# Optimization experiments

Hardware: AMD Instinct MI355X
Metric: run time of the kernel (lower is better)

Reference implementation:

```python
import jax, jax.numpy as jnp
import numpy as np

N, C, T, V, O, S, R = 32, 64, 256, 25, 192, 3, 8  # batch, in_ch, time, joints, out_ch, subsets, rel_ch


def setup_inputs() -> dict:
    key = jax.random.key(0)
    ks = jax.random.split(key, 20)
    w = lambda i, shape: (jax.random.normal(ks[i], shape, jnp.float32) * 0.05)
    return {
        "x": jax.random.normal(ks[0], (N, C, T, V), jnp.float32),
        "spd_A": jax.random.normal(ks[1], (V, V), jnp.float32) * 0.1,
        "A3": jax.random.normal(ks[2], (S, V, V), jnp.float32) * 0.1,
        "A6": jax.random.normal(ks[3], (6, V, V), jnp.float32) * 0.1,
        "conv1_w": w(4, (S, R, C)), "conv1_b": jnp.zeros((S, R), jnp.float32),
        "conv2_w": w(5, (S, R, C)), "conv2_b": jnp.zeros((S, R), jnp.float32),
        "conv4_w": w(6, (S, O, R)), "conv4_b": jnp.zeros((S, O), jnp.float32),
        "conv3_w": w(7, (S, O, C)), "conv3_b": jnp.zeros((S, O), jnp.float32),
        "alpha": jnp.full((1,), 0.5, jnp.float32),
        "beta": jnp.full((1,), 0.5, jnp.float32),
        "gamma": jnp.full((1,), 0.5, jnp.float32),
        "bn_w": jnp.ones((O,), jnp.float32), "bn_b": jnp.zeros((O,), jnp.float32),
        "down_w": w(8, (O, C)), "down_b": jnp.zeros((O,), jnp.float32),
        "dbn_w": jnp.ones((O,), jnp.float32), "dbn_b": jnp.zeros((O,), jnp.float32),
    }


def _bn(y, w, b):
    # BatchNorm2d in training mode: stats over (N, T, V) per channel, biased var
    mu = y.mean(axis=(0, 2, 3), keepdims=True)
    var = ((y - mu) ** 2).mean(axis=(0, 2, 3), keepdims=True)
    return (y - mu) * jax.lax.rsqrt(var + 1e-5) * w[None, :, None, None] + b[None, :, None, None]


def reference(x, spd_A, A3, A6, conv1_w, conv1_b, conv2_w, conv2_b, conv4_w, conv4_b,
              conv3_w, conv3_b, alpha, beta, gamma, bn_w, bn_b, down_w, down_b, dbn_w, dbn_b):
    out_c = conv4_w.shape[1]
    # A6 expanded: (out//6, 6, V, V) -> (out, V, V); contiguous-view == tile along channel blocks
    A6_ex = jnp.tile(A6, (out_c // 6, 1, 1))  # (O, V, V)
    # 1x1 conv then temporal mean == conv on temporal mean (linear op commutes)
    xm = x.mean(axis=2)  # (N, C, V)
    x1 = jnp.einsum('ncv,src->nsrv', xm, conv1_w) + conv1_b[None, :, :, None]
    x2 = jnp.einsum('ncv,src->nsrv', xm, conv2_w) + conv2_b[None, :, :, None]
    d = jnp.tanh(x1[..., :, None] - x2[..., None, :])  # (N, S, R, V, V)
    A_dyn = jnp.einsum('nsruv,sor->nsouv', d, conv4_w) + conv4_b[None, :, :, None, None]
    A_at = (A_dyn * alpha + A3[None, :, None, :, :]
            + A6_ex[None, None] * beta + spd_A[None, None, None] * gamma)  # (N, S, O, V, V)
    # CTRGC_2: x3 = conv3(x); einsum 'ncuv,nctv->nctu', summed over subsets
    x3 = jnp.einsum('nctv,soc->nsotv', x, conv3_w) + conv3_b[None, :, :, None, None]
    y = jnp.einsum('nsouv,nsotv->notu', A_at, x3)  # (N, O, T, V)
    y = _bn(y, bn_w, bn_b)
    xd = jnp.einsum('nctv,oc->notv', x, down_w) + down_b[None, :, None, None]
    y = jax.nn.relu(y + _bn(xd, dbn_w, dbn_b))
    return y
```

## Files before the change

kernel.cpp:

```cpp
#include <hip/hip_runtime.h>

#define N_ 32
#define C_ 64
#define T_ 256
#define V_ 25
#define O_ 192
#define S_ 3
#define R_ 8
#define VV (V_*V_)
#define TV (T_*V_)
#define RP 26
#define TRP (T_*RP)

typedef unsigned short u16;
typedef unsigned int u32;
typedef __attribute__((ext_vector_type(4))) u16 u16x4;
typedef __attribute__((ext_vector_type(8))) u16 u16x8;
typedef __attribute__((ext_vector_type(4))) u32 u32x4;
typedef __attribute__((ext_vector_type(8))) __bf16 bf16x8;
typedef __attribute__((ext_vector_type(4))) float f32x4;

#define WS_A2F_U 0
#define WS_XQ_U  (18874368)
#define WS_XD_U  (18874368 + 13631488)
#define WS_YB_U  (18874368 + 13631488 + 39321600)
#define WS_XM_F   (55574528)
#define WS_RS_F   (55574528 + 51200)
#define WS_STAT_F (55574528 + 51200 + 153600)
#define WS_COEF_F (55574528 + 51200 + 153600 + 768)

__device__ __forceinline__ u16 f2b(float f) {
    return __builtin_bit_cast(u16, (__bf16)f);
}
__device__ __forceinline__ float b2f(u16 u) {
    return __builtin_bit_cast(float, ((unsigned)u) << 16);
}
__device__ __forceinline__ f32x4 mfma16(bf16x8 a, bf16x8 b, f32x4 c) {
    return __builtin_amdgcn_mfma_f32_16x16x32_bf16(a, b, c, 0, 0, 0);
}

__global__ void k0_xq(const float* __restrict__ x, u16* __restrict__ xq) {
    __shared__ float tile[64][52];
    int bid = blockIdx.x;
    int n = bid >> 7, tb = bid & 127;
    int t0 = tb * 2;
    int tid = threadIdx.x;
    const float2* xp = (const float2*)(x + (size_t)n * C_ * TV + t0 * 25);
    for (int p = tid; p < 1600; p += 256) {
        int c = p / 25, q = p % 25;
        float2 f2 = xp[(size_t)c * 3200 + q];
        tile[c][q * 2] = f2.x;
        tile[c][q * 2 + 1] = f2.y;
    }
    __syncthreads();
    for (int p = tid; p < 832; p += 256) {
        int row = p >> 4, c4g = p & 15;
        int t = row >= RP, v = row - t * RP;
        u16x4 w;
        #pragma unroll
        for (int i = 0; i < 4; ++i) {
            int co = ((c4g & 3) << 4) + ((c4g >> 2) << 2) + i;
            w[i] = (v < 25) ? f2b(tile[co][t * 25 + v]) : (u16)0;
        }
        *(u16x4*)&xq[((size_t)n * TRP + tb * 52 + row) * 64 + c4g * 4] = w;
    }
}

__global__ void k1_xm(const u16* __restrict__ xq, float* __restrict__ xm_out) {
    __shared__ float ps[256];
    int bid = blockIdx.x;
    int n = bid / 25, v = bid % 25;
    int tid = threadIdx.x;
    int cg = tid & 63, tg = tid >> 6;
    const u16* p = xq + (size_t)n * TRP * 64 + ((size_t)(tg * 64 * RP + v)) * 64 + cg;
    float s = 0.f;
    for (int t = 0; t < 64; ++t) {
        s += b2f(*p);
        p += RP * 64;
    }
    ps[tid] = s;
    __syncthreads();
    if (tid < 64) {
        float tot = ps[tid] + ps[64 + tid] + ps[128 + tid] + ps[192 + tid];
        int c4g = tid >> 2, i = tid & 3;
        int co = ((c4g & 3) << 4) + ((c4g >> 2) << 2) + i;
        xm_out[((size_t)n * C_ + co) * V_ + v] = tot * (1.f / T_);
    }
}

__global__ void k2_a2f(const float* __restrict__ spd, const float* __restrict__ A3,
                       const float* __restrict__ A6,
                       const float* __restrict__ w1, const float* __restrict__ b1,
                       const float* __restrict__ w2, const float* __restrict__ b2,
                       const float* __restrict__ w4, const float* __restrict__ b4,
                       const float* __restrict__ b3,
                       const float* __restrict__ alpha, const float* __restrict__ beta,
                       const float* __restrict__ gamma,
                       u16* __restrict__ a2f, const float* __restrict__ xmbuf,
                       float* __restrict__ rs_tot) {
    __shared__ float xm[C_ * V_];
    __shared__ float x1s[R_ * V_], x2s[R_ * V_];
    __shared__ float dm[R_ * VV];
    __shared__ float a3s[VV], sps[VV], a6s[6 * VV];
    __shared__ float aat[2 * VV];
    __shared__ float w4s[2][R_];
    __shared__ float b4s[2];
    int bid = blockIdx.x;
    int n = bid / 24;
    int rem = bid % 24;
    int s = rem / 8, og = rem % 8;
    int tid = threadIdx.x;
    const float* xmg = xmbuf + (size_t)n * C_ * V_;
    for (int p = tid; p < C_ * V_; p += 256) xm[p] = xmg[p];
    for (int p = tid; p < VV; p += 256) { a3s[p] = A3[s * VV + p]; sps[p] = spd[p]; }
    for (int p = tid; p < 6 * VV; p += 256) a6s[p] = A6[p];
    __syncthreads();
    if (tid < R_ * V_) {
        int r = tid / V_, v = tid % V_;
        float acc1 = b1[s * R_ + r], acc2 = b2[s * R_ + r];
        for (int c = 0; c < C_; ++c) {
            float xv = xm[c * V_ + v];
            acc1 += xv * w1[(s * R_ + r) * C_ + c];
            acc2 += xv * w2[(s * R_ + r) * C_ + c];
        }
        x1s[tid] = acc1; x2s[tid] = acc2;
    }
    __syncthreads();
    for (int p = tid; p < R_ * VV; p += 256) {
        int r = p / VV, uv = p % VV, u = uv / V_, v = uv % V_;
        dm[p] = tanhf(x1s[r * V_ + u] - x2s[r * V_ + v]);
    }
    __syncthreads();
    float al = alpha[0], be = beta[0], ga = gamma[0];
    for (int op = 0; op < 12; ++op) {
        int o0 = og * 24 + op * 2;
        if (tid < 16) w4s[tid >> 3][tid & 7] =
            w4[((size_t)(s * O_ + o0 + (tid >> 3))) * R_ + (tid & 7)];
        if (tid < 2) b4s[tid] = b4[s * O_ + o0 + tid];
        __syncthreads();
        for (int p = tid; p < 2 * VV; p += 256) {
            int oo = p / VV, pp = p % VV;
            float acc = b4s[oo];
            #pragma unroll
            for (int r = 0; r < R_; ++r) acc += dm[r * VV + pp] * w4s[oo][r];
            int o = o0 + oo;
            aat[p] = al * acc + a3s[pp] + be * a6s[(o % 6) * VV + pp] + ga * sps[pp];
        }
        __syncthreads();
        if (tid < 2 * V_) {
            int oo = tid / V_, u = tid % V_;
            float rs = 0.f;
            for (int v = 0; v < V_; ++v) rs += aat[oo * VV + u * V_ + v];
            atomicAdd(&rs_tot[((size_t)(n * O_ + o0 + oo)) * V_ + u],
                      b3[s * O_ + o0 + oo] * rs);
        }
        {
            int oo = tid >> 7, l2 = tid & 127, cu = l2 >> 6, l = l2 & 63;
            int u = cu * 16 + (l & 15);
            u16x8 w;
            #pragma unroll
            for (int j = 0; j < 8; ++j) {
                int v = ((j >> 2) << 4) + ((l >> 4) << 2) + (j & 3);
                float val = 0.f;
                if (u < V_ && v < V_) val = aat[oo * VV + u * V_ + v];
                w[j] = f2b(val);
            }
            size_t idx = ((((size_t)(n * O_ + o0 + oo)) * S_ + s) * 2 + cu) * 64 + l;
            ((u16x8*)a2f)[idx] = w;
        }
        __syncthreads();
    }
}

#define OSTR_B 2504
#define SSTR_B 832
#define BUF_B  20064

__global__ __launch_bounds__(256, 3)
void k3_main(const u16* __restrict__ xq,
             const float* __restrict__ w3, const float* __restrict__ dw,
             const float* __restrict__ db,
             const u16* __restrict__ a2f, const float* __restrict__ rs_tot,
             u16* __restrict__ yb16, u16* __restrict__ xdws,
             float* __restrict__ stats) {
    __shared__ char x3Lb[2 * BUF_B];
    __shared__ u16 xdst[8 * 416];
    __shared__ u16 ystage[8 * 400];
    int orig = blockIdx.x;
    int bid = (orig & 7) * 96 + (orig >> 3);
    int n = bid / 24;
    int o0 = (bid % 24) * 8;
    int tid = threadIdx.x, wid = tid >> 6, lane = tid & 63;
    int lr = lane & 15, lg = lane >> 4;
    int colt = wid & 1;
    int rt0 = (wid >> 1) * 13;

    for (int p = tid; p < 2 * BUF_B / 16; p += 256) ((u32x4*)x3Lb)[p] = u32x4{0,0,0,0};

    const float* wsrc = (colt == 0)
        ? w3 + ((size_t)((lr >> 3) * O_ + o0 + (lr & 7))) * C_
        : ((lr < 8) ? w3 + ((size_t)(2 * O_ + o0 + lr)) * C_
                    : dw + ((size_t)(o0 + lr - 8)) * C_);
    bf16x8 bw[2];
    #pragma unroll
    for (int ks = 0; ks < 2; ++ks) {
        u16x8 tmp;
        #pragma unroll
        for (int j = 0; j < 8; ++j) {
            int c = ks * 32 + (lg << 2) + (j & 3) + ((j >> 2) << 4);
            tmp[j] = f2b(wsrc[c]);
        }
        bw[ks] = __builtin_bit_cast(bf16x8, tmp);
    }
    float dbv = (colt == 1 && lr >= 8) ? db[o0 + lr - 8] : 0.f;

    int wo = (colt == 0) ? (lr & 7) : lr;
    int wsb = (colt == 0) ? (lr >> 3) : 2;
    int colbyte = wo * OSTR_B + wsb * SSTR_B;

    const bf16x8* a2v = (const bf16x8*)a2f;
    bf16x8 Bh[2][6];
    float rsb0[2], rsb1[2];
    #pragma unroll
    for (int oi = 0; oi < 2; ++oi) {
        int o = o0 + (wid << 1) + oi;
        const bf16x8* bp = a2v + ((size_t)(n * O_ + o)) * 6 * 64 + lane;
        #pragma unroll
        for (int q = 0; q < 6; ++q) Bh[oi][q] = bp[(size_t)q * 64];
        const float* rsp = rs_tot + ((size_t)(n * O_ + o)) * V_;
        rsb0[oi] = rsp[lr];
        rsb1[oi] = (lr < 9) ? rsp[16 + lr] : 0.f;
    }

    float sy1[2] = {0, 0}, sy2[2] = {0, 0};
    float sd1 = 0.f, sd2 = 0.f;
    const u16* xbn = xq + (size_t)n * TRP * 64;
    int rdw = 13 * lr + 2 * lg;
    char* buf = x3Lb;
    int t0 = 0;

    auto tl = [&](int ch, int j, u16x8& A0, u16x8& A1) {
        const u16* p = xbn + ((size_t)(ch * 16) * RP + (size_t)((rt0 + j) * 16 + lr)) * 64
                       + (lg << 4);
        A0 = *(const u16x8*)p;
        A1 = *(const u16x8*)(p + 8);
    };
    auto proc = [&](int rt, u16x8 A0, u16x8 A1) {
        f32x4 acc = {0.f, 0.f, 0.f, 0.f};
        acc = mfma16(__builtin_bit_cast(bf16x8, A0), bw[0], acc);
        acc = mfma16(__builtin_bit_cast(bf16x8, A1), bw[1], acc);
        int rbase = rt * 16 + (lg << 2);
        if (colt == 0 || lr < 8) {
            u16x4 w;
            #pragma unroll
            for (int reg = 0; reg < 4; ++reg) w[reg] = f2b(acc[reg]);
            *(u16x4*)(buf + colbyte + rbase * 2) = w;
        } else {
            u16x4 w;
            #pragma unroll
            for (int reg = 0; reg < 4; ++reg) {
                int rr = rbase + reg;
                int t = rr / RP, v = rr - t * RP;
                float val = acc[reg] + dbv;
                w[reg] = f2b(val);
                if (v < 25) { sd1 += val; sd2 += val * val; }
            }
            *(u16x4*)&xdst[(lr - 8) * 416 + rbase] = w;
        }
    };

    __syncthreads();

    u16x8 p0a, p0b, p1a, p1b, p2a, p2b, p3a, p3b;
    tl(0, 0, p0a, p0b); tl(0, 1, p1a, p1b); tl(0, 2, p2a, p2b); tl(0, 3, p3a, p3b);

    for (int ch = 0; ch < 16; ++ch) {
        t0 = ch * 16;
        buf = x3Lb + (ch & 1) * BUF_B;
        proc(rt0 + 0, p0a, p0b);
        proc(rt0 + 1, p1a, p1b);
        proc(rt0 + 2, p2a, p2b);
        proc(rt0 + 3, p3a, p3b);
        for (int j = 4; j < 13; ++j) {
            u16x8 A0, A1;
            tl(ch, j, A0, A1);
            proc(rt0 + j, A0, A1);
        }
        if (ch < 15) {
            tl(ch + 1, 0, p0a, p0b); tl(ch + 1, 1, p1a, p1b);
            tl(ch + 1, 2, p2a, p2b); tl(ch + 1, 3, p3a, p3b);
        }
        __syncthreads();
        #pragma unroll
        for (int oi = 0; oi < 2; ++oi) {
            int ol = (wid << 1) + oi;
            const u32* L = (const u32*)(buf + ol * OSTR_B);
            f32x4 acc0 = {0, 0, 0, 0}, acc1 = {0, 0, 0, 0};
            #pragma unroll
            for (int s = 0; s < 3; ++s) {
                const u32* Ls = L + s * 208 + rdw;
                u32 d0 = Ls[0], d1 = Ls[1], d8 = Ls[8], d9 = Ls[9];
                bf16x8 A = __builtin_bit_cast(bf16x8, u32x4{d0, d1, d8, d9});
                acc0 = mfma16(A, Bh[oi][s * 2 + 0], acc0);
                acc1 = mfma16(A, Bh[oi][s * 2 + 1], acc1);
            }
            int ylb = ol * 400 + (lg << 2) * 25;
            #pragma unroll
            for (int reg = 0; reg < 4; ++reg) {
                float v0 = acc0[reg] + rsb0[oi];
                ystage[ylb + reg * 25 + lr] = f2b(v0);
                sy1[oi] += v0; sy2[oi] += v0 * v0;
                if (lr < 9) {
                    float v1 = acc1[reg] + rsb1[oi];
                    ystage[ylb + reg * 25 + 16 + lr] = f2b(v1);
                    sy1[oi] += v1; sy2[oi] += v1 * v1;
                }
            }
        }
        {
            size_t ygb = (size_t)(n * O_ + o0) * TV + (size_t)t0 * V_;
            for (int q = lane; q < 100; q += 64) {
                int sel = q >= 50;
                int ol2 = (wid << 1) + sel;
                int j = q - sel * 50;
                u16x8 pk = *(const u16x8*)&ystage[ol2 * 400 + j * 8];
                *(u16x8*)&yb16[ygb + (size_t)ol2 * TV + j * 8] = pk;
            }
        }
        if (colt == 1) {
            int tofs = (wid >> 1) * 8;
            size_t gdb = (size_t)(n * O_ + o0) * TV + (size_t)(t0 + tofs) * V_;
            for (int q = lane; q < 200; q += 64) {
                int o = q / 25, w = q - o * 25;
                int g0 = w * 8;
                int tl2 = g0 / 25, v = g0 - tl2 * 25;
                u16x8 pk;
                #pragma unroll
                for (int k = 0; k < 8; ++k) {
                    pk[k] = xdst[o * 416 + (tofs + tl2) * RP + v];
                    if (++v == 25) { v = 0; ++tl2; }
                }
                *(u16x8*)&xdws[gdb + (size_t)o * TV + g0] = pk;
            }
        }
    }
    #pragma unroll
    for (int oi = 0; oi < 2; ++oi) {
        float v1 = sy1[oi], v2 = sy2[oi];
        #pragma unroll
        for (int m = 1; m < 64; m <<= 1) {
            v1 += __shfl_xor(v1, m);
            v2 += __shfl_xor(v2, m);
        }
        if (lane == 0) {
            atomicAdd(&stats[0 * O_ + o0 + (wid << 1) + oi], v1);
            atomicAdd(&stats[1 * O_ + o0 + (wid << 1) + oi], v2);
        }
    }
    if (colt == 1) {
        float v1 = sd1, v2 = sd2;
        v1 += __shfl_xor(v1, 16); v2 += __shfl_xor(v2, 16);
        v1 += __shfl_xor(v1, 32); v2 += __shfl_xor(v2, 32);
        if (lane >= 8 && lane < 16) {
            atomicAdd(&stats[2 * O_ + o0 + lane - 8], v1);
            atomicAdd(&stats[3 * O_ + o0 + lane - 8], v2);
        }
    }
}

__global__ void k4_coef(const float* __restrict__ bn_w, const float* __restrict__ bn_b,
                        const float* __restrict__ dbn_w, const float* __restrict__ dbn_b,
                        const float* __restrict__ stats, float* __restrict__ coef) {
    int o = threadIdx.x;
    if (o >= O_) return;
    float inv = 1.f / (float)(N_ * T_ * V_);
    float mu_y = stats[o] * inv;
    float var_y = stats[O_ + o] * inv - mu_y * mu_y;
    float ay = bn_w[o] * rsqrtf(var_y + 1e-5f);
    float by = bn_b[o] - mu_y * ay;
    float mu_d = stats[2 * O_ + o] * inv;
    float var_d = stats[3 * O_ + o] * inv - mu_d * mu_d;
    float ad = dbn_w[o] * rsqrtf(var_d + 1e-5f);
    float bd = dbn_b[o] - mu_d * ad;
    coef[o] = ay; coef[O_ + o] = by; coef[2 * O_ + o] = ad; coef[3 * O_ + o] = bd;
}

__global__ void k5_final(float* __restrict__ out, const u16* __restrict__ yb,
                         const u16* __restrict__ xd, const float* __restrict__ cf) {
    size_t total = (size_t)N_ * O_ * TV / 8;
    for (size_t i = blockIdx.x * (size_t)blockDim.x + threadIdx.x; i < total;
         i += (size_t)gridDim.x * blockDim.x) {
        int o = (int)((i / 800) % O_);
        float ay = cf[o], by = cf[O_ + o], ad = cf[2 * O_ + o], bd = cf[3 * O_ + o];
        u16x8 yv = ((const u16x8*)yb)[i];
        u16x8 dv = ((const u16x8*)xd)[i];
        float4 r0, r1;
        r0.x = fmaxf(ay * b2f(yv[0]) + by + ad * b2f(dv[0]) + bd, 0.f);
        r0.y = fmaxf(ay * b2f(yv[1]) + by + ad * b2f(dv[1]) + bd, 0.f);
        r0.z = fmaxf(ay * b2f(yv[2]) + by + ad * b2f(dv[2]) + bd, 0.f);
        r0.w = fmaxf(ay * b2f(yv[3]) + by + ad * b2f(dv[3]) + bd, 0.f);
        r1.x = fmaxf(ay * b2f(yv[4]) + by + ad * b2f(dv[4]) + bd, 0.f);
        r1.y = fmaxf(ay * b2f(yv[5]) + by + ad * b2f(dv[5]) + bd, 0.f);
        r1.z = fmaxf(ay * b2f(yv[6]) + by + ad * b2f(dv[6]) + bd, 0.f);
        r1.w = fmaxf(ay * b2f(yv[7]) + by + ad * b2f(dv[7]) + bd, 0.f);
        ((float4*)out)[2 * i] = r0;
        ((float4*)out)[2 * i + 1] = r1;
    }
}

extern "C" void kernel_launch(void* const* d_in, const int* in_sizes, int n_in,
                              void* d_out, int out_size, void* d_ws, size_t ws_size,
                              hipStream_t stream) {
    const float* x     = (const float*)d_in[0];
    const float* spd   = (const float*)d_in[1];
    const float* A3    = (const float*)d_in[2];
    const float* A6    = (const float*)d_in[3];
    const float* w1    = (const float*)d_in[4];
    const float* b1    = (const float*)d_in[5];
    const float* w2    = (const float*)d_in[6];
    const float* b2    = (const float*)d_in[7];
    const float* w4    = (const float*)d_in[8];
    const float* b4    = (const float*)d_in[9];
    const float* w3    = (const float*)d_in[10];
    const float* b3    = (const float*)d_in[11];
    const float* alpha = (const float*)d_in[12];
    const float* beta  = (const float*)d_in[13];
    const float* gamma = (const float*)d_in[14];
    const float* bn_w  = (const float*)d_in[15];
    const float* bn_b  = (const float*)d_in[16];
    const float* dw    = (const float*)d_in[17];
    const float* db    = (const float*)d_in[18];
    const float* dbn_w = (const float*)d_in[19];
    const float* dbn_b = (const float*)d_in[20];
    float* out = (float*)d_out;
    u16*   wsu = (u16*)d_ws;
    float* wsf = (float*)d_ws;

    u16* a2f  = wsu + WS_A2F_U;
    u16* xq   = wsu + WS_XQ_U;
    u16* xd   = wsu + WS_XD_U;
    u16* yb   = wsu + WS_YB_U;
    float* xm    = wsf + WS_XM_F;
    float* rs    = wsf + WS_RS_F;
    float* stats = wsf + WS_STAT_F;
    float* coef  = wsf + WS_COEF_F;

    hipMemsetAsync(rs, 0, (N_ * O_ * V_ + 4 * O_) * sizeof(float), stream);

    k0_xq<<<N_ * 128, 256, 0, stream>>>(x, xq);
    k1_xm<<<N_ * 25, 256, 0, stream>>>(xq, xm);
    k2_a2f<<<N_ * S_ * 8, 256, 0, stream>>>(spd, A3, A6, w1, b1, w2, b2, w4, b4, b3,
                                            alpha, beta, gamma, a2f, xm, rs);
    k3_main<<<N_ * 24, 256, 0, stream>>>(xq, w3, dw, db, a2f, rs, yb, xd, stats);
    k4_coef<<<1, 256, 0, stream>>>(bn_w, bn_b, dbn_w, dbn_b, stats, coef);
    k5_final<<<4096, 256, 0, stream>>>(out, yb, xd, coef);
}
```

Baseline: 315.4 us.

## Split main kernel time range across two blocks and make a2f per-wave

```diff
diff --git a/kernel.cpp b/kernel.cpp
--- a/kernel.cpp
+++ b/kernel.cpp
@@ -101,19 +101,16 @@
     __shared__ float xm[C_ * V_];
     __shared__ float x1s[R_ * V_], x2s[R_ * V_];
     __shared__ float dm[R_ * VV];
-    __shared__ float a3s[VV], sps[VV], a6s[6 * VV];
-    __shared__ float aat[2 * VV];
-    __shared__ float w4s[2][R_];
-    __shared__ float b4s[2];
+    __shared__ float a3s[VV], sps[VV];
+    __shared__ float aatw[4][2 * VV];
     int bid = blockIdx.x;
     int n = bid / 24;
     int rem = bid % 24;
     int s = rem / 8, og = rem % 8;
-    int tid = threadIdx.x;
+    int tid = threadIdx.x, wid = tid >> 6, lane = tid & 63;
     const float* xmg = xmbuf + (size_t)n * C_ * V_;
     for (int p = tid; p < C_ * V_; p += 256) xm[p] = xmg[p];
     for (int p = tid; p < VV; p += 256) { a3s[p] = A3[s * VV + p]; sps[p] = spd[p]; }
-    for (int p = tid; p < 6 * VV; p += 256) a6s[p] = A6[p];
     __syncthreads();
     if (tid < R_ * V_) {
         int r = tid / V_, v = tid % V_;
@@ -132,30 +129,37 @@
     }
     __syncthreads();
     float al = alpha[0], be = beta[0], ga = gamma[0];
-    for (int op = 0; op < 12; ++op) {
+    float* aat = aatw[wid];
+    for (int opi = 0; opi < 3; ++opi) {
+        int op = wid * 3 + opi;
         int o0 = og * 24 + op * 2;
-        if (tid < 16) w4s[tid >> 3][tid & 7] =
-            w4[((size_t)(s * O_ + o0 + (tid >> 3))) * R_ + (tid & 7)];
-        if (tid < 2) b4s[tid] = b4[s * O_ + o0 + tid];
-        __syncthreads();
-        for (int p = tid; p < 2 * VV; p += 256) {
-            int oo = p / VV, pp = p % VV;
-            float acc = b4s[oo];
-            #pragma unroll
-            for (int r = 0; r < R_; ++r) acc += dm[r * VV + pp] * w4s[oo][r];
-            int o = o0 + oo;
-            aat[p] = al * acc + a3s[pp] + be * a6s[(o % 6) * VV + pp] + ga * sps[pp];
-        }
-        __syncthreads();
-        if (tid < 2 * V_) {
-            int oo = tid / V_, u = tid % V_;
+        float w4v[2][R_], b4v[2];
+        #pragma unroll
+        for (int oo = 0; oo < 2; ++oo) {
+            b4v[oo] = b4[s * O_ + o0 + oo];
+            #pragma unroll
+            for (int r = 0; r < R_; ++r)
+                w4v[oo][r] = w4[((size_t)(s * O_ + o0 + oo)) * R_ + r];
+        }
+        const float* a6p0 = A6 + ((o0 % 6) * VV);
+        for (int p = lane; p < 2 * VV; p += 64) {
+            int oo = p / VV, pp = p - oo * VV;
+            float acc = b4v[oo];
+            #pragma unroll
+            for (int r = 0; r < R_; ++r) acc += dm[r * VV + pp] * w4v[oo][r];
+            aat[p] = al * acc + a3s[pp] + ga * sps[pp] + be * a6p0[oo * VV + pp];
+        }
+        if (lane < 2 * V_) {
+            int oo = lane / V_, u = lane - oo * V_;
             float rs = 0.f;
             for (int v = 0; v < V_; ++v) rs += aat[oo * VV + u * V_ + v];
             atomicAdd(&rs_tot[((size_t)(n * O_ + o0 + oo)) * V_ + u],
                       b3[s * O_ + o0 + oo] * rs);
         }
-        {
-            int oo = tid >> 7, l2 = tid & 127, cu = l2 >> 6, l = l2 & 63;
+        #pragma unroll
+        for (int it = 0; it < 4; ++it) {
+            int idx = it * 64 + lane;
+            int oo = idx >> 7, l2 = idx & 127, cu = l2 >> 6, l = l2 & 63;
             int u = cu * 16 + (l & 15);
             u16x8 w;
             #pragma unroll
@@ -165,10 +169,9 @@
                 if (u < V_ && v < V_) val = aat[oo * VV + u * V_ + v];
                 w[j] = f2b(val);
             }
-            size_t idx = ((((size_t)(n * O_ + o0 + oo)) * S_ + s) * 2 + cu) * 64 + l;
-            ((u16x8*)a2f)[idx] = w;
-        }
-        __syncthreads();
+            size_t idxg = ((((size_t)(n * O_ + o0 + oo)) * S_ + s) * 2 + cu) * 64 + l;
+            ((u16x8*)a2f)[idxg] = w;
+        }
     }
 }
 
@@ -176,26 +179,28 @@
 #define SSTR_B 832
 #define BUF_B  20064
 
-__global__ __launch_bounds__(256, 3)
+__global__ __launch_bounds__(256, 4)
 void k3_main(const u16* __restrict__ xq,
              const float* __restrict__ w3, const float* __restrict__ dw,
              const float* __restrict__ db,
              const u16* __restrict__ a2f, const float* __restrict__ rs_tot,
              u16* __restrict__ yb16, u16* __restrict__ xdws,
              float* __restrict__ stats) {
-    __shared__ char x3Lb[2 * BUF_B];
+    __shared__ char x3Lb[BUF_B];
     __shared__ u16 xdst[8 * 416];
     __shared__ u16 ystage[8 * 400];
     int orig = blockIdx.x;
-    int bid = (orig & 7) * 96 + (orig >> 3);
-    int n = bid / 24;
-    int o0 = (bid % 24) * 8;
+    int bid = (orig & 7) * 192 + (orig >> 3);
+    int n = bid / 48;
+    int rem = bid % 48;
+    int o0 = (rem >> 1) * 8;
+    int th = rem & 1;
     int tid = threadIdx.x, wid = tid >> 6, lane = tid & 63;
     int lr = lane & 15, lg = lane >> 4;
     int colt = wid & 1;
     int rt0 = (wid >> 1) * 13;
 
-    for (int p = tid; p < 2 * BUF_B / 16; p += 256) ((u32x4*)x3Lb)[p] = u32x4{0,0,0,0};
+    for (int p = tid; p < BUF_B / 16; p += 256) ((u32x4*)x3Lb)[p] = u32x4{0,0,0,0};
 
     const float* wsrc = (colt == 0)
         ? w3 + ((size_t)((lr >> 3) * O_ + o0 + (lr & 7))) * C_
@@ -237,11 +242,10 @@
     const u16* xbn = xq + (size_t)n * TRP * 64;
     int rdw = 13 * lr + 2 * lg;
     char* buf = x3Lb;
-    int t0 = 0;
 
     auto tl = [&](int ch, int j, u16x8& A0, u16x8& A1) {
-        const u16* p = xbn + ((size_t)(ch * 16) * RP + (size_t)((rt0 + j) * 16 + lr)) * 64
-                       + (lg << 4);
+        const u16* p = xbn + ((size_t)((th * 128 + ch * 16)) * RP
+                              + (size_t)((rt0 + j) * 16 + lr)) * 64 + (lg << 4);
         A0 = *(const u16x8*)p;
         A1 = *(const u16x8*)(p + 8);
     };
@@ -274,9 +278,8 @@
     u16x8 p0a, p0b, p1a, p1b, p2a, p2b, p3a, p3b;
     tl(0, 0, p0a, p0b); tl(0, 1, p1a, p1b); tl(0, 2, p2a, p2b); tl(0, 3, p3a, p3b);
 
-    for (int ch = 0; ch < 16; ++ch) {
-        t0 = ch * 16;
-        buf = x3Lb + (ch & 1) * BUF_B;
+    for (int ch = 0; ch < 8; ++ch) {
+        int t0 = th * 128 + ch * 16;
         proc(rt0 + 0, p0a, p0b);
         proc(rt0 + 1, p1a, p1b);
         proc(rt0 + 2, p2a, p2b);
@@ -286,7 +289,7 @@
             tl(ch, j, A0, A1);
             proc(rt0 + j, A0, A1);
         }
-        if (ch < 15) {
+        if (ch < 7) {
             tl(ch + 1, 0, p0a, p0b); tl(ch + 1, 1, p1a, p1b);
             tl(ch + 1, 2, p2a, p2b); tl(ch + 1, 3, p3a, p3b);
         }
@@ -343,6 +346,7 @@
                 *(u16x8*)&xdws[gdb + (size_t)o * TV + g0] = pk;
             }
         }
+        __syncthreads();
     }
     #pragma unroll
     for (int oi = 0; oi < 2; ++oi) {
@@ -451,7 +455,7 @@
     k1_xm<<<N_ * 25, 256, 0, stream>>>(xq, xm);
     k2_a2f<<<N_ * S_ * 8, 256, 0, stream>>>(spd, A3, A6, w1, b1, w2, b2, w4, b4, b3,
                                             alpha, beta, gamma, a2f, xm, rs);
-    k3_main<<<N_ * 24, 256, 0, stream>>>(xq, w3, dw, db, a2f, rs, yb, xd, stats);
+    k3_main<<<N_ * 48, 256, 0, stream>>>(xq, w3, dw, db, a2f, rs, yb, xd, stats);
     k4_coef<<<1, 256, 0, stream>>>(bn_w, bn_b, dbn_w, dbn_b, stats, coef);
     k5_final<<<4096, 256, 0, stream>>>(out, yb, xd, coef);
 }
```

Measured after the change: 452.9 us. 1.44x slower.
